# Kernel tuning notes

Hardware: AMD Instinct MI355X
Metric: run time of the kernel (lower is better)

Reference implementation:

```python
import jax, jax.numpy as jnp
from jax import lax
import numpy as np

# Model dims (see shape_source)
D_MODEL = 768
N_LAYERS = 8
D_STATE = 16
EXPAND = 2
D_INNER = EXPAND * D_MODEL          # 1536
DT_RANK = (D_MODEL + 15) // 16       # 48
D_CONV = 4
PATCH = 16
IMG = 224
CH = 3
BATCH = 8


def rmsnorm(x, w, eps=1e-5):
    return x * lax.rsqrt(jnp.mean(x * x, axis=-1, keepdims=True) + eps) * w


def patch_embed(img, w, b):
    # img: [B,C,H,W] -> tokens [B, N, d_model]
    x = lax.conv_general_dilated(img, w, (PATCH, PATCH), 'VALID',
                                 dimension_numbers=('NCHW', 'OIHW', 'NCHW'))
    x = x + b[None, :, None, None]
    Bsz = img.shape[0]
    return x.reshape(Bsz, D_MODEL, -1).transpose(0, 2, 1)


def mamba_block(x, in_w, cw, cb, xw, dtw, dtb, a_log, d_p, ow):
    # x: [B, L, d_model]
    Bsz, L, _ = x.shape
    xz = x @ in_w.T                                   # [B,L,2*ED]
    xin, z = jnp.split(xz, 2, axis=-1)
    # causal depthwise conv over L
    xc = lax.conv_general_dilated(xin.transpose(0, 2, 1), cw, (1,),
                                  [(D_CONV - 1, 0)],
                                  dimension_numbers=('NCH', 'OIH', 'NCH'),
                                  feature_group_count=D_INNER)
    xin = jax.nn.silu((xc + cb[None, :, None]).transpose(0, 2, 1))  # [B,L,ED]
    dbc = xin @ xw.T                                  # [B,L,dt_rank+2N]
    delta, Bm, Cm = jnp.split(dbc, [DT_RANK, DT_RANK + D_STATE], axis=-1)
    delta = jax.nn.softplus(delta @ dtw.T + dtb)      # [B,L,ED]
    A = -jnp.exp(a_log)                               # [ED,N]
    dA = jnp.exp(delta[..., None] * A)                # [B,L,ED,N]
    dBx = (delta * xin)[..., None] * Bm[:, :, None, :]  # [B,L,ED,N]

    def step(h, inp):
        a, bx = inp
        h = a * h + bx
        return h, h

    h0 = jnp.zeros((Bsz, D_INNER, D_STATE), x.dtype)
    _, hs = lax.scan(step, h0, (dA.transpose(1, 0, 2, 3), dBx.transpose(1, 0, 2, 3)))
    y = jnp.einsum('lben,bln->ble', hs, Cm)           # [B,L,ED]
    y = y + d_p * xin
    y = y * jax.nn.silu(z)
    return y @ ow.T                                   # [B,L,d_model]


def setup_inputs() -> dict:
    key = jax.random.key(0)
    ks = jax.random.split(key, 16)
    s = 0.02
    nl = N_LAYERS
    inp = {
        'rgb': jax.random.normal(ks[0], (BATCH, CH, IMG, IMG), jnp.float32),
        't': jax.random.normal(ks[1], (BATCH, CH, IMG, IMG), jnp.float32),
        'pe_w': jax.random.normal(ks[2], (D_MODEL, CH, PATCH, PATCH), jnp.float32) * s,
        'pe_b': jnp.zeros((D_MODEL,), jnp.float32),
        'in_proj_w': jax.random.normal(ks[3], (nl, 2 * D_INNER, D_MODEL), jnp.float32) * s,
        'conv_w': jax.random.normal(ks[4], (nl, D_INNER, 1, D_CONV), jnp.float32) * s,
        'conv_b': jnp.zeros((nl, D_INNER), jnp.float32),
        'x_proj_w': jax.random.normal(ks[5], (nl, DT_RANK + 2 * D_STATE, D_INNER), jnp.float32) * s,
        'dt_proj_w': jax.random.normal(ks[6], (nl, D_INNER, DT_RANK), jnp.float32) * s,
        'dt_proj_b': jax.random.normal(ks[7], (nl, D_INNER), jnp.float32) * s,
        'A_log': jnp.log(jnp.broadcast_to(jnp.arange(1.0, D_STATE + 1.0), (nl, D_INNER, D_STATE))),
        'D': jnp.ones((nl, D_INNER), jnp.float32),
        'out_proj_w': jax.random.normal(ks[8], (nl, D_MODEL, D_INNER), jnp.float32) * s,
        'norm_w': jnp.ones((nl, D_MODEL), jnp.float32),
    }
    return inp


def reference(rgb, t, pe_w, pe_b, in_proj_w, conv_w, conv_b, x_proj_w,
              dt_proj_w, dt_proj_b, A_log, D, out_proj_w, norm_w):
    rt = patch_embed(rgb, pe_w, pe_b)   # [B,196,768]
    tt = patch_embed(t, pe_w, pe_b)
    x = jnp.concatenate([rt, tt], axis=1)  # [B,392,768]
    for i in range(N_LAYERS):
        x = x + mamba_block(rmsnorm(x, norm_w[i]), in_proj_w[i], conv_w[i],
                            conv_b[i], x_proj_w[i], dt_proj_w[i], dt_proj_b[i],
                            A_log[i], D[i], out_proj_w[i])
    Bsz = rgb.shape[0]
    # [B,2N,D] -> [B,2N,D,1] -> transpose(0,3) -> [1,2N,D,B] -> [2B,C,H,W]
    out = jnp.transpose(x[..., None], (3, 1, 2, 0)).reshape(2 * Bsz, CH, IMG, IMG)
    return out[:Bsz], out[Bsz:]
```

## Files before the change

### kernel.cpp

```cpp
#include <hip/hip_runtime.h>
#include <cstddef>
#include <cstdint>

#define L_TOK 392
#define BATCH 8
#define DM    768
#define ED    1536
#define NST   16
#define DTR   48
#define ROWS  (BATCH * L_TOK)

#define C_CH 8
#define CLEN 49
#define EGB  24

#define XP_Z  6


typedef unsigned short ushortT;
typedef __bf16 bf16x8 __attribute__((ext_vector_type(8)));
typedef unsigned short us8 __attribute__((ext_vector_type(8)));
typedef unsigned short us4 __attribute__((ext_vector_type(4)));
typedef float f32x4 __attribute__((ext_vector_type(4)));

#define LOG2E 1.4426950408889634f

__device__ __forceinline__ float bf2f(ushortT u) {
    union { unsigned int i; float f; } v; v.i = ((unsigned int)u) << 16; return v.f;
}
__device__ __forceinline__ ushortT f2bf(float f) {
    union { float f; unsigned int i; } v; v.f = f;
    unsigned int r = v.i + 0x7FFFu + ((v.i >> 16) & 1u);
    return (ushortT)(r >> 16);
}

enum { EPI_STORE = 0, EPI_BIAS = 1, EPI_BIAS_SOFTPLUS = 2, EPI_ADD = 3 };

__global__ __launch_bounds__(256)
void convert3_kernel(const float* __restrict__ s0, ushortT* __restrict__ d0, int n0,
                     const float* __restrict__ s1, ushortT* __restrict__ d1, int n1,
                     const float* __restrict__ s2, ushortT* __restrict__ d2, int n2)
{
    int idx = blockIdx.x * 256 + threadIdx.x;
    const float* s; ushortT* d;
    if (idx < n0) { s = s0; d = d0; }
    else if (idx < n0 + n1) { idx -= n0; s = s1; d = d1; }
    else if (idx < n0 + n1 + n2) { idx -= n0 + n1; s = s2; d = d2; }
    else return;
    float4 f = *(const float4*)(s + (size_t)idx * 4);
    us4 h; h.x = f2bf(f.x); h.y = f2bf(f.y); h.z = f2bf(f.z); h.w = f2bf(f.w);
    *(us4*)(d + (size_t)idx * 4) = h;
}

template <int EPI, bool C_BF, bool SPLIT, bool ATOMIC, bool PARTIAL>
__global__ __launch_bounds__(256)
void gemm_mfma(const ushortT* __restrict__ A, int lda,
               const ushortT* __restrict__ W, int ldw,
               const float* __restrict__ bias,
               void* __restrict__ Cv, void* __restrict__ Cv2, int ldc,
               int M, int N, int K, int kchunk)
{
    __shared__ ushortT As[2][128 * 40];
    __shared__ ushortT Ws[2][128 * 40];

    const int tid  = threadIdx.x;
    const int lane = tid & 63;
    const int wave = tid >> 6;
    const int wm   = wave >> 1;
    const int wn   = wave & 1;
    const int quad = lane >> 4;
    const int l16  = lane & 15;

    const int gx   = gridDim.x;
    const int nwg  = gx * gridDim.y;
    const int flat = blockIdx.y * gx + blockIdx.x;
    const int q = nwg >> 3, r = nwg & 7;
    const int xcd = flat & 7, sidx = flat >> 3;
    const int swz = (xcd < r ? xcd * (q + 1) : r * (q + 1) + (xcd - r) * q) + sidx;

    const int m0 = (swz / gx) * 128;
    const int n0 = (swz % gx) * 128;
    const int kb = blockIdx.z * kchunk;
    const int KT = kchunk / 32;

    const int ar    = tid >> 1;
    const int ahalf = tid & 1;

    const int gm_a = m0 + ar;
    const bool a_ok = gm_a < M;
    const ushortT* aptr = A + (size_t)gm_a * lda + ahalf * 16;
    const int gw_w = n0 + ar;
    const bool w_ok = gw_w < N;
    const ushortT* wptr = W + (size_t)gw_w * ldw + ahalf * 16;

    us8 a0A = {0,0,0,0,0,0,0,0}, a1A = {0,0,0,0,0,0,0,0};
    us8 w0A = {0,0,0,0,0,0,0,0}, w1A = {0,0,0,0,0,0,0,0};
    us8 a0B = {0,0,0,0,0,0,0,0}, a1B = {0,0,0,0,0,0,0,0};
    us8 w0B = {0,0,0,0,0,0,0,0}, w1B = {0,0,0,0,0,0,0,0};

    auto g_load = [&](int k0, us8& A0, us8& A1, us8& W0, us8& W1) {
        if (a_ok) {
            const ushortT* src = aptr + k0;
            A0 = *(const us8*)(src);
            A1 = *(const us8*)(src + 8);
        }
        if (w_ok) {
            const ushortT* src = wptr + k0;
            W0 = *(const us8*)(src);
            W1 = *(const us8*)(src + 8);
        }
    };
    auto l_store = [&](int buf, const us8& A0, const us8& A1,
                       const us8& W0, const us8& W1) {
        *(us8*)&As[buf][ar * 40 + ahalf * 16]     = A0;
        *(us8*)&As[buf][ar * 40 + ahalf * 16 + 8] = A1;
        *(us8*)&Ws[buf][ar * 40 + ahalf * 16]     = W0;
        *(us8*)&Ws[buf][ar * 40 + ahalf * 16 + 8] = W1;
    };

    f32x4 acc[4][4] = {};

    auto compute = [&](int buf) {
        bf16x8 af[4], bw[4];
#pragma unroll
        for (int t = 0; t < 4; ++t) {
            us8 ta = *(const us8*)&As[buf][(wm * 64 + t * 16 + l16) * 40 + quad * 8];
            af[t] = __builtin_bit_cast(bf16x8, ta);
            us8 tb = *(const us8*)&Ws[buf][(wn * 64 + t * 16 + l16) * 40 + quad * 8];
            bw[t] = __builtin_bit_cast(bf16x8, tb);
        }
#pragma unroll
        for (int i = 0; i < 4; ++i)
#pragma unroll
            for (int j = 0; j < 4; ++j)
                acc[i][j] = __builtin_amdgcn_mfma_f32_16x16x32_bf16(
                    af[i], bw[j], acc[i][j], 0, 0, 0);
    };

    g_load(kb, a0A, a1A, w0A, w1A);
    l_store(0, a0A, a1A, w0A, w1A);
    if (KT > 1) g_load(kb + 32, a0B, a1B, w0B, w1B);
    __syncthreads();

    for (int kt = 0; kt < KT; kt += 2) {
        if (kt + 2 < KT) g_load(kb + (kt + 2) * 32, a0A, a1A, w0A, w1A);
        compute(0);
        if (kt + 1 < KT) l_store(1, a0B, a1B, w0B, w1B);
        __syncthreads();
        if (kt + 1 >= KT) break;
        if (kt + 3 < KT) g_load(kb + (kt + 3) * 32, a0B, a1B, w0B, w1B);
        compute(1);
        if (kt + 2 < KT) l_store(0, a0A, a1A, w0A, w1A);
        __syncthreads();
    }

#pragma unroll
    for (int i = 0; i < 4; ++i) {
#pragma unroll
        for (int r2 = 0; r2 < 4; ++r2) {
            int gm = m0 + wm * 64 + i * 16 + quad * 4 + r2;
            if (gm >= M) continue;
#pragma unroll
            for (int j = 0; j < 4; ++j) {
                int gn = n0 + wn * 64 + j * 16 + l16;
                if (gn >= N) continue;
                float v = acc[i][j][r2];
                if (EPI == EPI_BIAS) v += bias[gn];
                void* dst = Cv;
                int cn = gn;
                if (SPLIT && gn >= ED) { dst = Cv2; cn = gn - ED; }
                size_t off = (size_t)gm * ldc + cn;
                if (PARTIAL) {
                    ((float*)dst)[(size_t)blockIdx.z * M * ldc + off] = v;
                } else if (ATOMIC) {
                    atomicAdd((float*)dst + off, v);
                } else if (C_BF) {
                    ((ushortT*)dst)[off] = f2bf(v);
                } else {
                    float* p = (float*)dst + off;
                    *p = (EPI == EPI_ADD) ? v + *p : v;
                }
            }
        }
    }
}

__global__ __launch_bounds__(256)
void reduce_partials_kernel(const float* __restrict__ P, float* __restrict__ dbc)
{
    int idx = blockIdx.x * 256 + threadIdx.x;
    if (idx >= ROWS * 80) return;
    float s = 0.f;
#pragma unroll
    for (int z = 0; z < XP_Z; ++z)
        s += P[(size_t)z * ROWS * 80 + idx];
    dbc[idx] = s;
}

template <int EPI, bool A_BF, bool C_BF>
__global__ __launch_bounds__(256)
void gemm_nt(const void* __restrict__ Av, int lda,
             const float* __restrict__ W, int ldw,
             const float* __restrict__ bias,
             void* __restrict__ Cv, int ldc,
             int M, int N, int K)
{
    __shared__ float As[16][68];
    __shared__ float Bs[16][68];
    const int tid = threadIdx.x;
    const int tx  = tid & 15;
    const int ty  = tid >> 4;
    const int bm  = blockIdx.y * 64;
    const int bn  = blockIdx.x * 64;
    const int lr  = tid >> 2;
    const int lk  = (tid & 3) * 4;

    float acc[4][4] = {};

    for (int k0 = 0; k0 < K; k0 += 16) {
        float a0 = 0.f, a1 = 0.f, a2 = 0.f, a3 = 0.f;
        float w0 = 0.f, w1 = 0.f, w2 = 0.f, w3 = 0.f;
        int ga = bm + lr;
        if (ga < M) {
            if (A_BF) {
                const ushortT* A = (const ushortT*)Av;
                ushort4 t = *(const ushort4*)(A + (size_t)ga * lda + k0 + lk);
                a0 = bf2f(t.x); a1 = bf2f(t.y); a2 = bf2f(t.z); a3 = bf2f(t.w);
            } else {
                const float* A = (const float*)Av;
                float4 t = *(const float4*)(A + (size_t)ga * lda + k0 + lk);
                a0 = t.x; a1 = t.y; a2 = t.z; a3 = t.w;
            }
        }
        int gw = bn + lr;
        if (gw < N) {
            float4 t = *(const float4*)(W + (size_t)gw * ldw + k0 + lk);
            w0 = t.x; w1 = t.y; w2 = t.z; w3 = t.w;
        }
        As[lk + 0][lr] = a0; As[lk + 1][lr] = a1;
        As[lk + 2][lr] = a2; As[lk + 3][lr] = a3;
        Bs[lk + 0][lr] = w0; Bs[lk + 1][lr] = w1;
        Bs[lk + 2][lr] = w2; Bs[lk + 3][lr] = w3;
        __syncthreads();
#pragma unroll
        for (int k = 0; k < 16; ++k) {
            float4 a4 = *(const float4*)&As[k][ty * 4];
            float4 b4 = *(const float4*)&Bs[k][tx * 4];
            float a[4] = {a4.x, a4.y, a4.z, a4.w};
            float b[4] = {b4.x, b4.y, b4.z, b4.w};
#pragma unroll
            for (int i = 0; i < 4; ++i)
#pragma unroll
                for (int j = 0; j < 4; ++j)
                    acc[i][j] += a[i] * b[j];
        }
        __syncthreads();
    }

#pragma unroll
    for (int i = 0; i < 4; ++i) {
        int gm = bm + ty * 4 + i;
        if (gm >= M) continue;
#pragma unroll
        for (int j = 0; j < 4; ++j) {
            int gn = bn + tx * 4 + j;
            if (gn >= N) continue;
            float v = acc[i][j];
            if (EPI == EPI_BIAS) v += bias[gn];
            if (EPI == EPI_BIAS_SOFTPLUS) {
                v += bias[gn];
                v = fmaxf(v, 0.f) + log1pf(expf(-fabsf(v)));
            }
            size_t off = (size_t)gm * ldc + gn;
            if (C_BF) {
                ((ushortT*)Cv)[off] = f2bf(v);
            } else {
                float* p = (float*)Cv + off;
                *p = (EPI == EPI_ADD) ? v + *p : v;
            }
        }
    }
}

__global__ __launch_bounds__(256)
void rmsnorm_kernel(const float* __restrict__ x, const float* __restrict__ w,
                    ushortT* __restrict__ xn)
{
    int r = blockIdx.x;
    const float* xr = x + (size_t)r * DM;
    float v[3];
    float s = 0.f;
#pragma unroll
    for (int i = 0; i < 3; ++i) {
        v[i] = xr[threadIdx.x + i * 256];
        s += v[i] * v[i];
    }
#pragma unroll
    for (int o = 32; o > 0; o >>= 1) s += __shfl_down(s, o, 64);
    __shared__ float wsum[4];
    __shared__ float scale_s;
    int wave = threadIdx.x >> 6;
    if ((threadIdx.x & 63) == 0) wsum[wave] = s;
    __syncthreads();
    if (threadIdx.x == 0) {
        float t = wsum[0] + wsum[1] + wsum[2] + wsum[3];
        scale_s = rsqrtf(t * (1.f / 768.f) + 1e-5f);
    }
    __syncthreads();
    float sc = scale_s;
#pragma unroll
    for (int i = 0; i < 3; ++i) {
        int d = threadIdx.x + i * 256;
        xn[(size_t)r * DM + d] = f2bf(v[i] * sc * w[d]);
    }
}

__global__ __launch_bounds__(256)
void conv_silu_kernel(const ushortT* __restrict__ xc, const float* __restrict__ cw,
                      const float* __restrict__ cb, ushortT* __restrict__ xin)
{
    int idx = blockIdx.x * 256 + threadIdx.x;
    if (idx >= ROWS * ED) return;
    int e = idx % ED;
    int r = idx / ED;
    int l = r % L_TOK;
    float w0 = cw[e * 4 + 0], w1 = cw[e * 4 + 1];
    float w2 = cw[e * 4 + 2], w3 = cw[e * 4 + 3];
    const ushortT* base = xc + (size_t)r * ED + e;
    float acc = cb[e] + w3 * bf2f(base[0]);
    if (l >= 1) acc += w2 * bf2f(base[-(ptrdiff_t)ED]);
    if (l >= 2) acc += w1 * bf2f(base[-(ptrdiff_t)(2 * ED)]);
    if (l >= 3) acc += w0 * bf2f(base[-(ptrdiff_t)(3 * ED)]);
    xin[(size_t)r * ED + e] = f2bf(acc / (1.f + __expf(-acc)));
}

__global__ __launch_bounds__(64)
void scan_part1(const ushortT* __restrict__ delta, const ushortT* __restrict__ xin,
                const float* __restrict__ dbc, const float* __restrict__ a_log,
                float* __restrict__ hend, float* __restrict__ sdl)
{
    __shared__ float BsL[CLEN * 16];
    const int tid = threadIdx.x;
    const int bid = blockIdx.x;
    const int eg = bid % EGB;
    const int c  = (bid / EGB) % C_CH;
    const int b  = bid / (EGB * C_CH);
    const int e  = eg * 64 + tid;
    const int l0 = c * CLEN;
    const int rb = b * L_TOK + l0;

    for (int i = tid; i < CLEN * 16; i += 64) {
        int s = i >> 4, n = i & 15;
        BsL[i] = dbc[(size_t)(rb + s) * 80 + 48 + n];
    }
    __syncthreads();

    float a[16];
    const float* ar = a_log + (size_t)e * 16;
#pragma unroll
    for (int n = 0; n < 16; ++n) a[n] = -__expf(ar[n]) * LOG2E;

    float h[16];
#pragma unroll
    for (int n = 0; n < 16; ++n) h[n] = 0.f;
    float sum_dl = 0.f;

    const size_t base = (size_t)rb * ED + e;
    float rdl[7], rxi[7];
#pragma unroll
    for (int j = 0; j < 7; ++j) {
        rdl[j] = bf2f(delta[base + (size_t)j * ED]);
        rxi[j] = bf2f(xin[base + (size_t)j * ED]);
    }
    for (int s0 = 0; s0 < CLEN; s0 += 7) {
#pragma unroll
        for (int j = 0; j < 7; ++j) {
            const int s = s0 + j;
            float dl = rdl[j], xi = rxi[j];
            int sp = s + 7; if (sp > CLEN - 1) sp = CLEN - 1;
            rdl[j] = bf2f(delta[base + (size_t)sp * ED]);
            rxi[j] = bf2f(xin[base + (size_t)sp * ED]);
            float dlxi = dl * xi;
            sum_dl += dl;
#pragma unroll
            for (int n = 0; n < 16; ++n)
                h[n] = __builtin_amdgcn_exp2f(dl * a[n]) * h[n] + dlxi * BsL[s * 16 + n];
        }
    }

    float* hp = hend + (((size_t)b * ED + e) * C_CH + c) * 16;
#pragma unroll
    for (int n = 0; n < 16; ++n) hp[n] = h[n];
    sdl[((size_t)b * ED + e) * C_CH + c] = sum_dl;
}

__global__ __launch_bounds__(64)
void scan_part2(const ushortT* __restrict__ delta, const ushortT* __restrict__ xin,
                const float* __restrict__ dbc, const ushortT* __restrict__ zb,
                const float* __restrict__ a_log, const float* __restrict__ dvec,
                const float* __restrict__ hend, const float* __restrict__ sdl,
                ushortT* __restrict__ y)
{
    __shared__ float BsL[CLEN * 16];
    __shared__ float CsL[CLEN * 16];
    const int tid = threadIdx.x;
    const int bid = blockIdx.x;
    const int eg = bid % EGB;
    const int c  = (bid / EGB) % C_CH;
    const int b  = bid / (EGB * C_CH);
    const int e  = eg * 64 + tid;
    const int l0 = c * CLEN;
    const int rb = b * L_TOK + l0;

    for (int i = tid; i < CLEN * 16; i += 64) {
        int s = i >> 4, n = i & 15;
        size_t row = (size_t)(rb + s) * 80;
        BsL[i] = dbc[row + 48 + n];
        CsL[i] = dbc[row + 64 + n];
    }
    __syncthreads();

    float a[16];
    const float* ar = a_log + (size_t)e * 16;
#pragma unroll
    for (int n = 0; n < 16; ++n) a[n] = -__expf(ar[n]) * LOG2E;
    const float dcf = dvec[e];

    float h[16];
#pragma unroll
    for (int n = 0; n < 16; ++n) h[n] = 0.f;
    const float* hb = hend + (((size_t)b * ED + e) * C_CH) * 16;
    const float* sb = sdl + ((size_t)b * ED + e) * C_CH;
    for (int cc = 0; cc < c; ++cc) {
        float sv = sb[cc];
#pragma unroll
        for (int n = 0; n < 16; ++n)
            h[n] = __builtin_amdgcn_exp2f(a[n] * sv) * h[n] + hb[cc * 16 + n];
    }

    const size_t base = (size_t)rb * ED + e;
    float rdl[7], rxi[7], rz[7];
#pragma unroll
    for (int j = 0; j < 7; ++j) {
        rdl[j] = bf2f(delta[base + (size_t)j * ED]);
        rxi[j] = bf2f(xin[base + (size_t)j * ED]);
        rz[j]  = bf2f(zb[base + (size_t)j * ED]);
    }
    for (int s0 = 0; s0 < CLEN; s0 += 7) {
#pragma unroll
        for (int j = 0; j < 7; ++j) {
            const int s = s0 + j;
            float dl = rdl[j], xi = rxi[j], z = rz[j];
            int sp = s + 7; if (sp > CLEN - 1) sp = CLEN - 1;
            rdl[j] = bf2f(delta[base + (size_t)sp * ED]);
            rxi[j] = bf2f(xin[base + (size_t)sp * ED]);
            rz[j]  = bf2f(zb[base + (size_t)sp * ED]);
            float dlxi = dl * xi;
            float yv = 0.f;
#pragma unroll
            for (int n = 0; n < 16; ++n) {
                h[n] = __builtin_amdgcn_exp2f(dl * a[n]) * h[n] + dlxi * BsL[s * 16 + n];
                yv += h[n] * CsL[s * 16 + n];
            }
            yv += dcf * xi;
            float sz = z / (1.f + __expf(-z));
            y[base + (size_t)s * ED] = f2bf(yv * sz);
        }
    }
}

__global__ __launch_bounds__(256)
void im2col_kernel(const float* __restrict__ rgb, const float* __restrict__ timg,
                   ushortT* __restrict__ P)
{
    int idx = blockIdx.x * 256 + threadIdx.x;
    if (idx >= ROWS * DM) return;
    int k = idx % DM;
    int r = idx / DM;
    int b = r / L_TOK;
    int l = r % L_TOK;
    const float* img = (l < 196) ? rgb : timg;
    int p  = (l < 196) ? l : l - 196;
    int py = p / 14, px = p % 14;
    int c  = k >> 8;
    int ph = (k >> 4) & 15;
    int pw = k & 15;
    P[idx] = f2bf(img[(((size_t)b * 3 + c) * 224 + (py * 16 + ph)) * 224 + (px * 16 + pw)]);
}

__global__ __launch_bounds__(256)
void out_transpose_kernel(const float* __restrict__ x, float* __restrict__ out)
{
    int idx = blockIdx.x * 256 + threadIdx.x;
    if (idx >= ROWS * DM) return;
    int b = idx & 7;
    int d = (idx >> 3) % DM;
    int l = idx / (8 * DM);
    out[idx] = x[((size_t)(b * L_TOK + l)) * DM + d];
}

extern "C" void kernel_launch(void* const* d_in, const int* in_sizes, int n_in,
                              void* d_out, int out_size, void* d_ws, size_t ws_size,
                              hipStream_t stream)
{
    (void)in_sizes; (void)n_in; (void)out_size; (void)ws_size;

    const float* rgb  = (const float*)d_in[0];
    const float* timg = (const float*)d_in[1];
    const float* pe_w = (const float*)d_in[2];
    const float* pe_b = (const float*)d_in[3];
    const float* in_w = (const float*)d_in[4];
    const float* cw   = (const float*)d_in[5];
    const float* cb   = (const float*)d_in[6];
    const float* xw   = (const float*)d_in[7];
    const float* dtw  = (const float*)d_in[8];
    const float* dtb  = (const float*)d_in[9];
    const float* alog = (const float*)d_in[10];
    const float* dvec = (const float*)d_in[11];
    const float* ow   = (const float*)d_in[12];
    const float* nw   = (const float*)d_in[13];

    char* p = (char*)d_ws;
    float*   X   = (float*)p;    p += (size_t)ROWS * DM * 4;
    ushortT* XC  = (ushortT*)p;  p += (size_t)ROWS * ED * 2;
    ushortT* Zb  = (ushortT*)p;  p += (size_t)ROWS * ED * 2;
    ushortT* XIN = (ushortT*)p;  p += (size_t)ROWS * ED * 2;
    ushortT* DEL = (ushortT*)p;  p += (size_t)ROWS * ED * 2;
    float*   DBC = (float*)p;    p += (size_t)ROWS * 80 * 4;
    ushortT* XN  = DEL;

    ushortT* INWB = XIN;
    ushortT* XWB  = (ushortT*)DBC;
    ushortT* PEB  = Zb;

    float* POUT = (float*)d_out;
    float* HEND = (float*)d_out;
    float* SDL  = HEND + (size_t)BATCH * ED * C_CH * 16;
    ushortT* OWB = (ushortT*)((char*)d_out +
                   ((size_t)BATCH * ED * C_CH * 16 + (size_t)BATCH * ED * C_CH) * 4);

    dim3 b256(256);
    const int MT = (ROWS + 127) / 128;
    const int SCAN_BLOCKS = BATCH * C_CH * EGB;

    const int PE_F4  = DM * DM / 4;
    const int INW_F4 = 2 * ED * DM / 4;
    const int XW_F4  = 80 * ED / 4;
    const int OW_F4  = DM * ED / 4;
    const int CVT_BLOCKS = (INW_F4 + XW_F4 + OW_F4 + 255) / 256;

    convert3_kernel<<<(PE_F4 + 255) / 256, b256, 0, stream>>>(
        pe_w, PEB, PE_F4, nullptr, nullptr, 0, nullptr, nullptr, 0);
    im2col_kernel<<<(ROWS * DM + 255) / 256, b256, 0, stream>>>(rgb, timg, XC);
    gemm_mfma<EPI_BIAS, false, false, false, false><<<dim3(DM / 128, MT), b256, 0, stream>>>(
        XC, DM, PEB, DM, pe_b, X, nullptr, DM, ROWS, DM, DM, DM);

    for (int i = 0; i < 8; ++i) {
        const float* in_wi = in_w + (size_t)i * 2 * ED * DM;
        const float* cwi   = cw   + (size_t)i * ED * 4;
        const float* cbi   = cb   + (size_t)i * ED;
        const float* xwi   = xw   + (size_t)i * 80 * ED;
        const float* dtwi  = dtw  + (size_t)i * ED * DTR;
        const float* dtbi  = dtb  + (size_t)i * ED;
        const float* ali   = alog + (size_t)i * ED * NST;
        const float* dvi   = dvec + (size_t)i * ED;
        const float* owi   = ow   + (size_t)i * DM * ED;
        const float* nwi   = nw   + (size_t)i * DM;

        convert3_kernel<<<CVT_BLOCKS, b256, 0, stream>>>(
            in_wi, INWB, INW_F4, xwi, XWB, XW_F4, owi, OWB, OW_F4);
        rmsnorm_kernel<<<ROWS, b256, 0, stream>>>(X, nwi, XN);
        gemm_mfma<EPI_STORE, true, true, false, false><<<dim3(2 * ED / 128, MT), b256, 0, stream>>>(
            XN, DM, INWB, DM, nullptr, XC, Zb, ED, ROWS, 2 * ED, DM, DM);
        conv_silu_kernel<<<(ROWS * ED + 255) / 256, b256, 0, stream>>>(
            XC, cwi, cbi, XIN);
        gemm_mfma<EPI_STORE, false, false, false, true><<<dim3(1, MT, XP_Z), b256, 0, stream>>>(
            XIN, ED, XWB, ED, nullptr, POUT, nullptr, 80, ROWS, 80, ED, ED / XP_Z);
        reduce_partials_kernel<<<(ROWS * 80 + 255) / 256, b256, 0, stream>>>(
            POUT, DBC);
        gemm_nt<EPI_BIAS_SOFTPLUS, false, true><<<dim3(ED / 64, ROWS / 64), b256, 0, stream>>>(
            DBC, 80, dtwi, DTR, dtbi, DEL, ED, ROWS, ED, DTR);
        scan_part1<<<SCAN_BLOCKS, 64, 0, stream>>>(
            DEL, XIN, DBC, ali, HEND, SDL);
        scan_part2<<<SCAN_BLOCKS, 64, 0, stream>>>(
            DEL, XIN, DBC, Zb, ali, dvi, HEND, SDL, XC);
        gemm_mfma<EPI_ADD, false, false, true, false><<<dim3(DM / 128, MT, 2), b256, 0, stream>>>(
            XC, ED, OWB, ED, nullptr, X, nullptr, DM, ROWS, DM, ED, ED / 2);
    }

    out_transpose_kernel<<<(ROWS * DM + 255) / 256, b256, 0, stream>>>(
        X, (float*)d_out);
}
```

Baseline: 1.956 ms.

## Stage GEMM tiles with direct global-to-LDS loads instead of register staging

The bf16 MFMA GEMM now fills its double-buffered shared-memory tiles with `global_load_lds` 16-byte transfers, one row segment per wave. Tiles go straight to LDS instead of through registers and explicit LDS stores. The main loop becomes a simple one-tile-ahead ping-pong with a single barrier per k-step. To fit the DMA layout the LDS row padding is dropped (stride 40 down to 32), which may bring back bank conflicts on the fragment reads. The row bounds checks are also removed, so edge tiles can read past M or N.

```diff
diff --git a/kernel.cpp b/kernel.cpp
--- a/kernel.cpp
+++ b/kernel.cpp
@@ -32,6 +32,12 @@
     union { float f; unsigned int i; } v; v.f = f;
     unsigned int r = v.i + 0x7FFFu + ((v.i >> 16) & 1u);
     return (ushortT)(r >> 16);
+}
+
+__device__ __forceinline__ void gload16(const void* g, void* l) {
+    __builtin_amdgcn_global_load_lds(
+        (const __attribute__((address_space(1))) void*)g,
+        (__attribute__((address_space(3))) void*)l, 16, 0, 0);
 }
 
 enum { EPI_STORE = 0, EPI_BIAS = 1, EPI_BIAS_SOFTPLUS = 2, EPI_ADD = 3 };
@@ -60,8 +66,8 @@
                void* __restrict__ Cv, void* __restrict__ Cv2, int ldc,
                int M, int N, int K, int kchunk)
 {
-    __shared__ ushortT As[2][128 * 40];
-    __shared__ ushortT Ws[2][128 * 40];
+    __shared__ ushortT As[2][128 * 32];
+    __shared__ ushortT Ws[2][128 * 32];
 
     const int tid  = threadIdx.x;
     const int lane = tid & 63;
@@ -83,39 +89,18 @@
     const int kb = blockIdx.z * kchunk;
     const int KT = kchunk / 32;
 
-    const int ar    = tid >> 1;
-    const int ahalf = tid & 1;
-
-    const int gm_a = m0 + ar;
-    const bool a_ok = gm_a < M;
-    const ushortT* aptr = A + (size_t)gm_a * lda + ahalf * 16;
-    const int gw_w = n0 + ar;
-    const bool w_ok = gw_w < N;
-    const ushortT* wptr = W + (size_t)gw_w * ldw + ahalf * 16;
-
-    us8 a0A = {0,0,0,0,0,0,0,0}, a1A = {0,0,0,0,0,0,0,0};
-    us8 w0A = {0,0,0,0,0,0,0,0}, w1A = {0,0,0,0,0,0,0,0};
-    us8 a0B = {0,0,0,0,0,0,0,0}, a1B = {0,0,0,0,0,0,0,0};
-    us8 w0B = {0,0,0,0,0,0,0,0}, w1B = {0,0,0,0,0,0,0,0};
-
-    auto g_load = [&](int k0, us8& A0, us8& A1, us8& W0, us8& W1) {
-        if (a_ok) {
-            const ushortT* src = aptr + k0;
-            A0 = *(const us8*)(src);
-            A1 = *(const us8*)(src + 8);
-        }
-        if (w_ok) {
-            const ushortT* src = wptr + k0;
-            W0 = *(const us8*)(src);
-            W1 = *(const us8*)(src + 8);
-        }
-    };
-    auto l_store = [&](int buf, const us8& A0, const us8& A1,
-                       const us8& W0, const us8& W1) {
-        *(us8*)&As[buf][ar * 40 + ahalf * 16]     = A0;
-        *(us8*)&As[buf][ar * 40 + ahalf * 16 + 8] = A1;
-        *(us8*)&Ws[buf][ar * 40 + ahalf * 16]     = W0;
-        *(us8*)&Ws[buf][ar * 40 + ahalf * 16 + 8] = W1;
+    const int srow = lane >> 2;
+    const int scol = (lane & 3) * 8;
+    const ushortT* aBase = A + (size_t)(m0 + srow) * lda + scol;
+    const ushortT* wBase = W + (size_t)(n0 + srow) * ldw + scol;
+
+    auto stage = [&](int buf, int k0) {
+#pragma unroll
+        for (int c = 0; c < 2; ++c) {
+            const int seg = wave * 2 + c;
+            gload16(aBase + (size_t)(seg * 16) * lda + k0, &As[buf][seg * 512]);
+            gload16(wBase + (size_t)(seg * 16) * ldw + k0, &Ws[buf][seg * 512]);
+        }
     };
 
     f32x4 acc[4][4] = {};
@@ -124,9 +109,9 @@
         bf16x8 af[4], bw[4];
 #pragma unroll
         for (int t = 0; t < 4; ++t) {
-            us8 ta = *(const us8*)&As[buf][(wm * 64 + t * 16 + l16) * 40 + quad * 8];
+            us8 ta = *(const us8*)&As[buf][(wm * 64 + t * 16 + l16) * 32 + quad * 8];
             af[t] = __builtin_bit_cast(bf16x8, ta);
-            us8 tb = *(const us8*)&Ws[buf][(wn * 64 + t * 16 + l16) * 40 + quad * 8];
+            us8 tb = *(const us8*)&Ws[buf][(wn * 64 + t * 16 + l16) * 32 + quad * 8];
             bw[t] = __builtin_bit_cast(bf16x8, tb);
         }
 #pragma unroll
@@ -137,20 +122,12 @@
                     af[i], bw[j], acc[i][j], 0, 0, 0);
     };
 
-    g_load(kb, a0A, a1A, w0A, w1A);
-    l_store(0, a0A, a1A, w0A, w1A);
-    if (KT > 1) g_load(kb + 32, a0B, a1B, w0B, w1B);
+    stage(0, kb);
     __syncthreads();
 
-    for (int kt = 0; kt < KT; kt += 2) {
-        if (kt + 2 < KT) g_load(kb + (kt + 2) * 32, a0A, a1A, w0A, w1A);
-        compute(0);
-        if (kt + 1 < KT) l_store(1, a0B, a1B, w0B, w1B);
-        __syncthreads();
-        if (kt + 1 >= KT) break;
-        if (kt + 3 < KT) g_load(kb + (kt + 3) * 32, a0B, a1B, w0B, w1B);
-        compute(1);
-        if (kt + 2 < KT) l_store(0, a0A, a1A, w0A, w1A);
+    for (int kt = 0; kt < KT; ++kt) {
+        if (kt + 1 < KT) stage((kt & 1) ^ 1, kb + (kt + 1) * 32);
+        compute(kt & 1);
         __syncthreads();
     }
 
```

Measured after the change: 1.733 ms. 11.4% less time.
